# Kernel optimization log

Measured on AMD Instinct MI355X. Metric: run time of the kernel, lower is better.

Reference implementation:

```python
import jax, jax.numpy as jnp
import numpy as np

B, L, D, H = 2, 2048, 2048, 16
DH = D // H  # 128 per-head dim
EPS = 1e-5


def setup_inputs() -> dict:
    key = jax.random.key(0)
    ks = jax.random.split(key, 6)
    s = 0.02  # xavier-ish init scale with gain 2**-2.5
    return {
        "hidden_states": jax.random.normal(ks[0], (B, L, D), jnp.float32),
        "Wq": jax.random.normal(ks[1], (D, D), jnp.float32) * s,
        "Wk": jax.random.normal(ks[2], (D, D), jnp.float32) * s,
        "Wv": jax.random.normal(ks[3], (D, D), jnp.float32) * s,
        "Wb": jax.random.normal(ks[4], (D, H), jnp.float32) * s,
        "o_norm_weight": jnp.ones((DH,), jnp.float32),
        "Wo": jax.random.normal(ks[5], (D, D), jnp.float32) * s,
    }


def _delta_rule(q, k, v, beta):
    """Recurrent delta-rule linear attention.
    q,k,v: [B,H,L,Dh]; beta: [B,H,L]. Math identical to fused_chunk_delta_rule.
    S_t = S_{t-1} + k_t (beta_t * (v_t - S_{t-1}^T k_t))^T ;  o_t = S_t^T q_t
    """
    def step(S, inp):
        qt, kt, vt, bt = inp  # [B,H,Dh],[B,H,Dh],[B,H,Dh],[B,H]
        v_pred = jnp.einsum('bhk,bhkv->bhv', kt, S)
        delta = (vt - v_pred) * bt[..., None]
        S = S + kt[..., None] * delta[:, :, None, :]
        ot = jnp.einsum('bhk,bhkv->bhv', qt, S)
        return S, ot

    xs = (q.transpose(2, 0, 1, 3), k.transpose(2, 0, 1, 3),
          v.transpose(2, 0, 1, 3), beta.transpose(2, 0, 1))
    S0 = jnp.zeros(q.shape[:2] + (q.shape[-1], v.shape[-1]), q.dtype)
    _, o = jax.lax.scan(step, S0, xs)  # o: [L,B,H,Dh]
    return o.transpose(1, 2, 0, 3)  # [B,H,L,Dh]


def reference(hidden_states, Wq, Wk, Wv, Wb, o_norm_weight, Wo):
    b, l, d = hidden_states.shape
    h = Wb.shape[1]
    dh = d // h

    q = hidden_states @ Wq
    k = hidden_states @ Wk
    v = jax.nn.silu(hidden_states @ Wv)

    def heads(x):
        return x.reshape(b, l, h, dh).transpose(0, 2, 1, 3)  # b h l d

    q, k, v = heads(q), heads(k), heads(v)

    # qk_norm = 'l2' (torch F.normalize with eps clamp)
    def l2n(x):
        n = jnp.sqrt(jnp.sum(x * x, axis=-1, keepdims=True))
        return x / jnp.maximum(n, 1e-12)

    q, k = l2n(q), l2n(k)
    q = q * (dh ** -0.5)  # fla delta-rule default scale

    beta = jax.nn.sigmoid(hidden_states @ Wb).transpose(0, 2, 1)  # b h l

    o = _delta_rule(q, k, v, beta)  # b h l dh
    o = o.transpose(0, 2, 1, 3)  # b l h dh

    # RMSNorm over head_v_dim
    o = o * jax.lax.rsqrt(jnp.mean(o * o, axis=-1, keepdims=True) + EPS)
    o = o * o_norm_weight

    return o.reshape(b, l, d) @ Wo
```

## Files before the change

### kernel.cpp

```cpp
#include <hip/hip_runtime.h>
#include <hip/hip_bf16.h>
#include <cstdint>

#define DEV static __device__ __forceinline__

typedef unsigned short u16;
typedef unsigned int u32;
typedef __attribute__((ext_vector_type(8))) short short8;
typedef __attribute__((ext_vector_type(4))) float f32x4;

constexpr int Bn = 2, Ln = 2048, Dn = 2048, Hn = 16;
constexpr int Mrows = Bn * Ln;
constexpr int CHK = 64, NCK = Ln / CHK;
constexpr int NCHUNKS = Bn * Hn * NCK;

DEV float b2f(u16 s) { union { float f; u32 u; } x; x.u = ((u32)s) << 16; return x.f; }
DEV u16 f2b(float f) {
  union { float f; u32 u; } x; x.f = f; u32 u = x.u;
  return (u16)((u + 0x7fffu + ((u >> 16) & 1u)) >> 16);
}

DEV void cp16(const void* g, void* l) {
  __builtin_amdgcn_global_load_lds(
      (const __attribute__((address_space(1))) u32*)(unsigned long long)(g),
      (__attribute__((address_space(3))) u32*)(unsigned long long)(l), 16, 0, 0);
}

DEV f32x4 mfma16(short8 a, short8 b, f32x4 c) {
  return __builtin_amdgcn_mfma_f32_16x16x32_bf16(a, b, c, 0, 0, 0);
}

__global__ void k_cvt(const float* __restrict__ src, u16* __restrict__ dst, int n8) {
  int i = blockIdx.x * blockDim.x + threadIdx.x;
  if (i >= n8) return;
  const float4* s4 = (const float4*)(src + (size_t)i * 8);
  float4 a = s4[0], b = s4[1];
  u16 o[8] = {f2b(a.x), f2b(a.y), f2b(a.z), f2b(a.w), f2b(b.x), f2b(b.y), f2b(b.z), f2b(b.w)};
  *(short8*)(dst + (size_t)i * 8) = *(short8*)o;
}

struct TransArgs {
  const float* src[5]; u16* dst[5]; int rows[5]; int cols[5];
};
__global__ void k_trans(TransArgs t) {
  __shared__ u16 tile[32][33];
  int z = blockIdx.z;
  const float* src = t.src[z]; u16* dst = t.dst[z];
  int rows = t.rows[z], cols = t.cols[z];
  int r0 = blockIdx.y * 32, c0 = blockIdx.x * 32;
  if (r0 >= rows || c0 >= cols) return;
  int tx = threadIdx.x, ty = threadIdx.y;
  for (int i = ty; i < 32; i += 8) {
    int r = r0 + i, c = c0 + tx;
    if (r < rows && c < cols) tile[i][tx] = f2b(src[(size_t)r * cols + c]);
  }
  __syncthreads();
  for (int i = ty; i < 32; i += 8) {
    int r = c0 + i, c = r0 + tx;
    if (r < cols && c < rows) dst[(size_t)r * rows + c] = tile[tx][i];
  }
}

__global__ __launch_bounds__(256) void k_beta(const u16* __restrict__ hs,
                                              const u16* __restrict__ WbT,
                                              float* __restrict__ beta_g) {
  __shared__ float part[256];
  int tid = threadIdx.x, wave = tid >> 6, lane = tid & 63, quad = lane >> 4, l15 = lane & 15;
  int tok0 = blockIdx.x * 16;
  const u16* arow = hs + (size_t)(tok0 + l15) * Dn + wave * 512;
  const u16* brow = WbT + (size_t)l15 * Dn + wave * 512;
  f32x4 acc = {0.f, 0.f, 0.f, 0.f};
#pragma unroll
  for (int k = 0; k < 512; k += 32) {
    short8 af = *(const short8*)&arow[k + quad * 8];
    short8 bf = *(const short8*)&brow[k + quad * 8];
    acc = mfma16(af, bf, acc);
  }
  part[tid] = 0.f;
  __syncthreads();
#pragma unroll
  for (int r = 0; r < 4; r++) atomicAdd(&part[l15 * 16 + quad * 4 + r], acc[r]);
  __syncthreads();
  int h = tid >> 4, tr = tid & 15;
  int b = tok0 >> 11;
  int l = (tok0 + tr) & 2047;
  beta_g[(size_t)(b * Hn + h) * Ln + l] = 1.f / (1.f + __expf(-part[h * 16 + tr]));
}

struct Gemm2Args { const u16* A; const u16* Bt; u16* C; int K; };

__global__ __launch_bounds__(512, 2) void k_gemm2(Gemm2Args g) {
  __shared__ u16 ldsbuf[61440];
  const char* LB = (const char*)ldsbuf;
  const int K = g.K, NT = K / 64;
  const size_t Kb = (size_t)K * 2;
  int tid = threadIdx.x, wave = tid >> 6, lane = tid & 63;
  int quad = lane >> 4, l15 = lane & 15;
  int wm = wave >> 2, wn = wave & 3;

  int bid = blockIdx.x;
  int wg = (bid & 7) * 32 + (bid >> 3);
  int by = wg >> 4, bx = wg & 15;
  int m0 = by * 256, n0f = bx * 384;

  int r0 = tid >> 2;
  int cby = (((tid & 3) ^ ((tid >> 3) & 3)) * 16);
  const char* gA = (const char*)g.A + (size_t)(m0 + r0) * Kb + cby;
  const char* gB = (const char*)g.Bt + (size_t)(n0f + r0) * Kb + cby;

  auto stageA = [&](int slot, int t, int kh) {
    const char* src = gA + (size_t)t * 128 + kh * 64;
    u16* dst = &ldsbuf[slot * 8192 + tid * 8];
    cp16(src, dst);
    cp16(src + (size_t)128 * Kb, dst + 4096);
  };
  auto stageB = [&](int slot, int t, int kh) {
    const char* src = gB + (size_t)t * 128 + kh * 64;
    u16* dst = &ldsbuf[24576 + slot * 12288 + tid * 8];
    cp16(src, dst);
    cp16(src + (size_t)128 * Kb, dst + 4096);
    cp16(src + (size_t)256 * Kb, dst + 8192);
  };

  f32x4 acc0[4][6], acc1[4][6];
#pragma unroll
  for (int i = 0; i < 4; i++)
#pragma unroll
    for (int j = 0; j < 6; j++) {
      acc0[i][j] = (f32x4){0.f, 0.f, 0.f, 0.f};
      acc1[i][j] = (f32x4){0.f, 0.f, 0.f, 0.f};
    }

  int rsw = (l15 >> 1) & 3;
  int rA = (wm * 128 + l15) * 64 + ((quad ^ rsw) * 16);
  int rB = (wn * 96 + l15) * 64 + ((quad ^ rsw) * 16);

  stageA(0, 0, 0);
  stageB(0, 0, 0);
  stageA(1, 0, 1);
  stageB(1, 0, 1);

  short8 bf[6];
  int u0 = 0;
  for (int t = 0; t < NT; ++t) {
    int u1 = u0 + 1; if (u1 == 3) u1 = 0;
    int u2 = u1 + 1; if (u2 == 3) u2 = 0;
    bool pf = (t + 1 < NT);
    const char* aK0 = LB + u0 * 16384;
    const char* aK1 = LB + u1 * 16384;
    const char* bK0 = LB + 49152 + u0 * 24576;
    const char* bK1 = LB + 49152 + u1 * 24576;

    asm volatile("s_waitcnt vmcnt(5)" ::: "memory");
    __builtin_amdgcn_s_barrier();
    __builtin_amdgcn_sched_barrier(0);
    if (pf) stageA(u2, t + 1, 0);
    {
      short8 av[4];
#pragma unroll
      for (int i = 0; i < 4; i++) av[i] = *(const short8*)(aK0 + rA + i * 1024);
#pragma unroll
      for (int j = 0; j < 6; j++) bf[j] = *(const short8*)(bK0 + rB + j * 1024);
      __builtin_amdgcn_s_setprio(1);
#pragma unroll
      for (int i = 0; i < 4; i++)
#pragma unroll
        for (int j = 0; j < 6; j++) acc0[i][j] = mfma16(av[i], bf[j], acc0[i][j]);
      __builtin_amdgcn_s_setprio(0);
    }

    asm volatile("s_waitcnt vmcnt(5)" ::: "memory");
    __builtin_amdgcn_s_barrier();
    __builtin_amdgcn_sched_barrier(0);
    if (pf) stageB(u2, t + 1, 0);
    {
      short8 av[4];
#pragma unroll
      for (int i = 0; i < 4; i++) av[i] = *(const short8*)(aK0 + rA + 4096 + i * 1024);
      __builtin_amdgcn_s_setprio(1);
#pragma unroll
      for (int i = 0; i < 4; i++)
#pragma unroll
        for (int j = 0; j < 6; j++) acc1[i][j] = mfma16(av[i], bf[j], acc1[i][j]);
      __builtin_amdgcn_s_setprio(0);
    }

    if (t == NT - 1) asm volatile("s_waitcnt vmcnt(0)" ::: "memory");
    else asm volatile("s_waitcnt vmcnt(5)" ::: "memory");
    __builtin_amdgcn_s_barrier();
    __builtin_amdgcn_sched_barrier(0);
    if (pf) stageA(u0, t + 1, 1);
    {
      short8 av[4];
#pragma unroll
      for (int i = 0; i < 4; i++) av[i] = *(const short8*)(aK1 + rA + i * 1024);
#pragma unroll
      for (int j = 0; j < 6; j++) bf[j] = *(const short8*)(bK1 + rB + j * 1024);
      __builtin_amdgcn_s_setprio(1);
#pragma unroll
      for (int i = 0; i < 4; i++)
#pragma unroll
        for (int j = 0; j < 6; j++) acc0[i][j] = mfma16(av[i], bf[j], acc0[i][j]);
      __builtin_amdgcn_s_setprio(0);
    }

    asm volatile("s_waitcnt vmcnt(5)" ::: "memory");
    __builtin_amdgcn_s_barrier();
    __builtin_amdgcn_sched_barrier(0);
    if (pf) stageB(u0, t + 1, 1);
    {
      short8 av[4];
#pragma unroll
      for (int i = 0; i < 4; i++) av[i] = *(const short8*)(aK1 + rA + 4096 + i * 1024);
      __builtin_amdgcn_s_setprio(1);
#pragma unroll
      for (int i = 0; i < 4; i++)
#pragma unroll
        for (int j = 0; j < 6; j++) acc1[i][j] = mfma16(av[i], bf[j], acc1[i][j]);
      __builtin_amdgcn_s_setprio(0);
    }

    u0 = u2;
  }

#pragma unroll
  for (int mq = 0; mq < 2; mq++) {
#pragma unroll
    for (int i = 0; i < 4; i++)
#pragma unroll
      for (int j = 0; j < 6; j++) {
        f32x4 a = mq ? acc1[i][j] : acc0[i][j];
        int row = m0 + wm * 128 + mq * 64 + i * 16 + quad * 4;
        int colg = n0f + wn * 96 + j * 16;
        int z = colg >> 11;
        u16* Cz = g.C + (size_t)z * ((size_t)Mrows * 2048);
        int col = (colg & 2047) + l15;
#pragma unroll
        for (int r = 0; r < 4; r++) {
          float v = a[r];
          if (z == 2) v = v / (1.f + __expf(-v));
          Cz[(size_t)(row + r) * 2048 + col] = f2b(v);
        }
      }
  }
}

struct GemmoArgs { const u16* A; const u16* Bt; float* C; int K; };

__global__ __launch_bounds__(512, 2) void k_gemmo(GemmoArgs g) {
  __shared__ u16 ldsbuf[36864];
  const char* LB = (const char*)ldsbuf;
  const int K = g.K, NT = K / 64;
  const size_t Kb = (size_t)K * 2;
  int tid = threadIdx.x, wave = tid >> 6, lane = tid & 63;
  int quad = lane >> 4, l15 = lane & 15;
  int wm = wave >> 2, wn = wave & 3;

  int bid = blockIdx.x;
  int wg = (bid & 7) * 32 + (bid >> 3);
  int bx = wg >> 5, by = wg & 31;
  int m0 = by * 128, n0 = bx * 256;

  int r0 = tid >> 2;
  int cby = (((tid & 3) ^ ((tid >> 3) & 3)) * 16);
  const char* gA = (const char*)g.A + (size_t)(m0 + r0) * Kb + cby;
  const char* gB = (const char*)g.Bt + (size_t)(n0 + r0) * Kb + cby;

  auto stageA = [&](int slot, int t, int kh) {
    const char* src = gA + (size_t)t * 128 + kh * 64;
    cp16(src, &ldsbuf[slot * 4096 + tid * 8]);
  };
  auto stageB = [&](int slot, int t, int kh) {
    const char* src = gB + (size_t)t * 128 + kh * 64;
    u16* dst = &ldsbuf[12288 + slot * 8192 + tid * 8];
    cp16(src, dst);
    cp16(src + (size_t)128 * Kb, dst + 4096);
  };

  f32x4 acc[4][4];
#pragma unroll
  for (int i = 0; i < 4; i++)
#pragma unroll
    for (int j = 0; j < 4; j++) acc[i][j] = (f32x4){0.f, 0.f, 0.f, 0.f};

  int rsw = (l15 >> 1) & 3;
  int rA = (wm * 64 + l15) * 64 + ((quad ^ rsw) * 16);
  int rB = (wn * 64 + l15) * 64 + ((quad ^ rsw) * 16);

  stageA(0, 0, 0);
  stageB(0, 0, 0);
  stageA(1, 0, 1);
  stageB(1, 0, 1);

  short8 av[4];
  int u0 = 0;
  for (int t = 0; t < NT; ++t) {
    int u1 = u0 + 1; if (u1 == 3) u1 = 0;
    int u2 = u1 + 1; if (u2 == 3) u2 = 0;
    bool pf = (t + 1 < NT);
    const char* aK0 = LB + u0 * 8192;
    const char* aK1 = LB + u1 * 8192;
    const char* bK0 = LB + 24576 + u0 * 16384;
    const char* bK1 = LB + 24576 + u1 * 16384;

    asm volatile("s_waitcnt vmcnt(3)" ::: "memory");
    __builtin_amdgcn_s_barrier();
    __builtin_amdgcn_sched_barrier(0);
    if (pf) stageA(u2, t + 1, 0);
    {
      short8 bv[2];
#pragma unroll
      for (int i = 0; i < 4; i++) av[i] = *(const short8*)(aK0 + rA + i * 1024);
#pragma unroll
      for (int j = 0; j < 2; j++) bv[j] = *(const short8*)(bK0 + rB + j * 1024);
      __builtin_amdgcn_s_setprio(1);
#pragma unroll
      for (int i = 0; i < 4; i++)
#pragma unroll
        for (int j = 0; j < 2; j++) acc[i][j] = mfma16(av[i], bv[j], acc[i][j]);
      __builtin_amdgcn_s_setprio(0);
    }

    asm volatile("s_waitcnt vmcnt(3)" ::: "memory");
    __builtin_amdgcn_s_barrier();
    __builtin_amdgcn_sched_barrier(0);
    if (pf) stageB(u2, t + 1, 0);
    {
      short8 bv[2];
#pragma unroll
      for (int j = 0; j < 2; j++) bv[j] = *(const short8*)(bK0 + rB + (2 + j) * 1024);
      __builtin_amdgcn_s_setprio(1);
#pragma unroll
      for (int i = 0; i < 4; i++)
#pragma unroll
        for (int j = 0; j < 2; j++) acc[i][2 + j] = mfma16(av[i], bv[j], acc[i][2 + j]);
      __builtin_amdgcn_s_setprio(0);
    }

    if (t == NT - 1) asm volatile("s_waitcnt vmcnt(0)" ::: "memory");
    else asm volatile("s_waitcnt vmcnt(3)" ::: "memory");
    __builtin_amdgcn_s_barrier();
    __builtin_amdgcn_sched_barrier(0);
    if (pf) stageA(u0, t + 1, 1);
    {
      short8 bv[2];
#pragma unroll
      for (int i = 0; i < 4; i++) av[i] = *(const short8*)(aK1 + rA + i * 1024);
#pragma unroll
      for (int j = 0; j < 2; j++) bv[j] = *(const short8*)(bK1 + rB + j * 1024);
      __builtin_amdgcn_s_setprio(1);
#pragma unroll
      for (int i = 0; i < 4; i++)
#pragma unroll
        for (int j = 0; j < 2; j++) acc[i][j] = mfma16(av[i], bv[j], acc[i][j]);
      __builtin_amdgcn_s_setprio(0);
    }

    asm volatile("s_waitcnt vmcnt(3)" ::: "memory");
    __builtin_amdgcn_s_barrier();
    __builtin_amdgcn_sched_barrier(0);
    if (pf) stageB(u0, t + 1, 1);
    {
      short8 bv[2];
#pragma unroll
      for (int j = 0; j < 2; j++) bv[j] = *(const short8*)(bK1 + rB + (2 + j) * 1024);
      __builtin_amdgcn_s_setprio(1);
#pragma unroll
      for (int i = 0; i < 4; i++)
#pragma unroll
        for (int j = 0; j < 2; j++) acc[i][2 + j] = mfma16(av[i], bv[j], acc[i][2 + j]);
      __builtin_amdgcn_s_setprio(0);
    }

    u0 = u2;
  }

#pragma unroll
  for (int i = 0; i < 4; i++)
#pragma unroll
    for (int j = 0; j < 4; j++) {
      int row = m0 + wm * 64 + i * 16 + quad * 4;
      int col = n0 + wn * 64 + j * 16 + l15;
#pragma unroll
      for (int r = 0; r < 4; r++)
        g.C[(size_t)(row + r) * 2048 + col] = acc[i][j][r];
    }
}

__global__ void k_l2(u16* qn, u16* kn) {
  int tid = threadIdx.x, wave = tid >> 6, lane = tid & 63;
  size_t row = (size_t)blockIdx.x * 4 + wave;
  u16* p = (blockIdx.y ? kn : qn) + row * 128;
  u32 u = *(const u32*)&p[lane * 2];
  float x0 = b2f((u16)(u & 0xffff)), x1 = b2f((u16)(u >> 16));
  float ss = x0 * x0 + x1 * x1;
#pragma unroll
  for (int o = 32; o > 0; o >>= 1) ss += __shfl_xor(ss, o, 64);
  float sc = 1.f / fmaxf(sqrtf(ss), 1e-12f);
  if (blockIdx.y == 0) sc *= 0.08838834764831845f;
  u32 outv = (u32)f2b(x0 * sc) | ((u32)f2b(x1 * sc) << 16);
  *(u32*)&p[lane * 2] = outv;
}

constexpr int ST = 72;
__global__ __launch_bounds__(256, 4) void k_pre(
    const float* __restrict__ beta_g,
    const u16* __restrict__ qn, const u16* __restrict__ kn, const u16* __restrict__ vn,
    u16* __restrict__ W2g, u16* __restrict__ Ug, u16* __restrict__ Gg, u16* __restrict__ KTg) {
  __shared__ float beta_s[64];
  __shared__ u16 mats[4 * 64 * ST];
  int gid = blockIdx.x;
  int c = gid & 31, h = (gid >> 5) & 15, b = gid >> 9;
  int tid = threadIdx.x;
  int l0 = c * 64;

  if (tid < 64) beta_s[tid] = beta_g[(size_t)(b * Hn + h) * Ln + l0 + tid];
  __syncthreads();

  int wave = tid >> 6, lane = tid & 63, quad = lane >> 4, l15 = lane & 15;
  u16 *Br = mats, *Bc = mats + 64 * ST, *M0 = mats + 2 * 64 * ST, *M1 = mats + 3 * 64 * ST;

  {
    const u16* krowB = kn + (size_t)(b * Ln + l0 + wave * 16 + l15) * Dn + h * 128;
    short8 bfr[4];
#pragma unroll
    for (int s = 0; s < 4; s++) bfr[s] = *(const short8*)&krowB[quad * 8 + 32 * s];
#pragma unroll
    for (int mt = 0; mt < 4; ++mt) {
      const u16* arow_k = kn + (size_t)(b * Ln + l0 + mt * 16 + l15) * Dn + h * 128;
      const u16* arow_q = qn + (size_t)(b * Ln + l0 + mt * 16 + l15) * Dn + h * 128;
      f32x4 accA = {0.f, 0.f, 0.f, 0.f}, accG = {0.f, 0.f, 0.f, 0.f};
#pragma unroll
      for (int s = 0; s < 4; s++) {
        short8 ak = *(const short8*)&arow_k[quad * 8 + 32 * s];
        short8 aq = *(const short8*)&arow_q[quad * 8 + 32 * s];
        accA = mfma16(ak, bfr[s], accA);
        accG = mfma16(aq, bfr[s], accG);
      }
      int t = wave * 16 + l15;
#pragma unroll
      for (int r = 0; r < 4; r++) {
        int i = mt * 16 + quad * 4 + r;
        u16 nb = f2b((t < i) ? -beta_s[i] * accA[r] : 0.f);
        Br[i * ST + t] = nb;
        Bc[t * ST + i] = nb;
        M0[i * ST + t] = (t == i) ? f2b(1.f) : nb;
        Gg[(size_t)gid * 4096 + (size_t)i * 64 + t] = f2b((t <= i) ? accG[r] : 0.f);
      }
    }
  }
  __syncthreads();

  u16 *Mc = M0, *Mn = M1;
#pragma unroll
  for (int it = 0; it < 5; ++it) {
    const int tT = (it < 3) ? 0 : ((it == 3) ? 1 : 2);
    const int tI = (it < 4) ? 0 : 1;
    short8 bb[2];
#pragma unroll
    for (int s = 0; s < 2; s++) bb[s] = *(const short8*)&Bc[(wave * 16 + l15) * ST + quad * 8 + 32 * s];
    f32x4 accT[4];
#pragma unroll
    for (int mt = 0; mt < 4; mt++) {
      accT[mt] = (f32x4){0.f, 0.f, 0.f, 0.f};
      if (mt - wave >= tT) {
#pragma unroll
        for (int s = 0; s < 2; s++) {
          short8 af = *(const short8*)&Br[(mt * 16 + l15) * ST + quad * 8 + 32 * s];
          accT[mt] = mfma16(af, bb[s], accT[mt]);
        }
      }
    }
    __syncthreads();
#pragma unroll
    for (int mt = 0; mt < 4; mt++) {
      if (mt - wave >= tI) {
#pragma unroll
        for (int r = 0; r < 4; r++) {
          int i = mt * 16 + quad * 4 + r, t = wave * 16 + l15;
          u16 v = f2b(accT[mt][r]);
          Br[i * ST + t] = v;
          Bc[t * ST + i] = v;
        }
      }
    }
    __syncthreads();
    short8 tb[2];
#pragma unroll
    for (int s = 0; s < 2; s++) tb[s] = *(const short8*)&Bc[(wave * 16 + l15) * ST + quad * 8 + 32 * s];
#pragma unroll
    for (int mt = 0; mt < 4; mt++) {
      if (mt - wave >= tT) {
        f32x4 a;
#pragma unroll
        for (int r = 0; r < 4; r++) a[r] = b2f(Mc[(mt * 16 + quad * 4 + r) * ST + wave * 16 + l15]);
#pragma unroll
        for (int s = 0; s < 2; s++) {
          short8 af = *(const short8*)&Mc[(mt * 16 + l15) * ST + quad * 8 + 32 * s];
          a = mfma16(af, tb[s], a);
        }
#pragma unroll
        for (int r = 0; r < 4; r++) Mn[(mt * 16 + quad * 4 + r) * ST + wave * 16 + l15] = f2b(a[r]);
      } else {
#pragma unroll
        for (int r = 0; r < 4; r++)
          Mn[(mt * 16 + quad * 4 + r) * ST + wave * 16 + l15] =
              Mc[(mt * 16 + quad * 4 + r) * ST + wave * 16 + l15];
      }
    }
    u16* tmp = Mc; Mc = Mn; Mn = tmp;
  }
  __syncthreads();

  u16* XT = mats;
  u16* Mb = Mn;
  for (int idx = tid; idx < 512; idx += 256) {
    int i = idx >> 3, t8 = (idx & 7) * 8;
    short8 m8 = *(const short8*)&Mc[i * ST + t8];
    short8 o8;
#pragma unroll
    for (int e = 0; e < 8; e++) o8[e] = (short)f2b(b2f((u16)m8[e]) * beta_s[t8 + e]);
    *(short8*)&Mb[i * ST + t8] = o8;
  }
  int tv = tid & 63, dk0 = (tid >> 6) * 32;
  for (int pass = 0; pass < 2; ++pass) {
    const u16* src = pass ? vn : kn;
    const u16* srow = src + (size_t)(b * Ln + l0 + tv) * Dn + h * 128 + dk0;
#pragma unroll
    for (int s = 0; s < 4; s++) {
      short8 vv = *(const short8*)&srow[s * 8];
#pragma unroll
      for (int e = 0; e < 8; e++) XT[(dk0 + s * 8 + e) * ST + tv] = (u16)vv[e];
    }
    __syncthreads();
    if (pass == 0) {
#pragma unroll
      for (int it2 = 0; it2 < 4; it2++) {
        int idx = tid + it2 * 256;
        int dk = idx >> 3, t0 = (idx & 7) * 8;
        *(short8*)&KTg[(size_t)gid * 8192 + dk * 64 + t0] =
            *(const short8*)&XT[dk * ST + t0];
      }
    }
    u16* dst = pass ? Ug : W2g;
#pragma unroll
    for (int half = 0; half < 2; ++half) {
      int nt = wave + half * 4;
      short8 bx[2];
#pragma unroll
      for (int s = 0; s < 2; s++) bx[s] = *(const short8*)&XT[(nt * 16 + l15) * ST + quad * 8 + 32 * s];
#pragma unroll
      for (int mt = 0; mt < 4; mt++) {
        f32x4 a = {0.f, 0.f, 0.f, 0.f};
#pragma unroll
        for (int s = 0; s < 2; s++) {
          short8 af = *(const short8*)&Mb[(mt * 16 + l15) * ST + quad * 8 + 32 * s];
          a = mfma16(af, bx[s], a);
        }
#pragma unroll
        for (int r = 0; r < 4; r++)
          dst[(size_t)gid * 8192 + (size_t)(mt * 16 + quad * 4 + r) * 128 + nt * 16 + l15] = f2b(a[r]);
      }
    }
    __syncthreads();
  }
}

struct Frg { short8 w2[4], qf[4], gf[2], k0[2], k1[2]; float u[4]; };

__global__ __launch_bounds__(256) void k_scan(
    const u16* __restrict__ qn, const u16* __restrict__ W2g, const u16* __restrict__ Ug,
    const u16* __restrict__ Gg, const u16* __restrict__ KTg, u16* __restrict__ Og) {
  constexpr int SST = 136, DST = 104;
  __shared__ u16 Sb[16 * SST];
  __shared__ u16 Db[16 * DST];
  int bh = blockIdx.x, sl = blockIdx.y;
  int b = bh >> 4, h = bh & 15, c0 = sl * 16;
  int tid = threadIdx.x, wave = tid >> 6, lane = tid & 63, quad = lane >> 4, l15 = lane & 15;
  for (int i = tid; i < 16 * SST; i += 256) Sb[i] = 0;
  f32x4 accS0 = {0.f, 0.f, 0.f, 0.f}, accS1 = {0.f, 0.f, 0.f, 0.f};
  __syncthreads();

  auto load_frags = [&](Frg& F, int ci) {
    size_t ck = (size_t)bh * NCK + ci;
    const u16* w2row = W2g + ck * 8192 + (size_t)(wave * 16 + l15) * 128;
    const u16* qrow = qn + (size_t)(b * Ln + ci * 64 + wave * 16 + l15) * Dn + h * 128;
#pragma unroll
    for (int s = 0; s < 4; s++) {
      F.w2[s] = *(const short8*)&w2row[quad * 8 + 32 * s];
      F.qf[s] = *(const short8*)&qrow[quad * 8 + 32 * s];
    }
    const u16* grow = Gg + ck * 4096 + (size_t)(wave * 16 + l15) * 64;
    const u16* kt0 = KTg + ck * 8192 + (size_t)(wave * 16 + l15) * 64;
    const u16* kt1 = KTg + ck * 8192 + (size_t)((wave + 4) * 16 + l15) * 64;
#pragma unroll
    for (int s = 0; s < 2; s++) {
      F.gf[s] = *(const short8*)&grow[quad * 8 + 32 * s];
      F.k0[s] = *(const short8*)&kt0[quad * 8 + 32 * s];
      F.k1[s] = *(const short8*)&kt1[quad * 8 + 32 * s];
    }
    const u16* urow = Ug + ck * 8192 + (size_t)(wave * 16 + quad * 4) * 128 + c0 + l15;
#pragma unroll
    for (int r = 0; r < 4; r++) F.u[r] = b2f(urow[(size_t)r * 128]);
  };

  auto compute = [&](const Frg& F, int ci) {
    f32x4 accT = {0.f, 0.f, 0.f, 0.f}, accO = {0.f, 0.f, 0.f, 0.f};
#pragma unroll
    for (int s = 0; s < 4; s++) {
      short8 sf = *(const short8*)&Sb[l15 * SST + quad * 8 + 32 * s];
      accT = mfma16(F.w2[s], sf, accT);
      accO = mfma16(F.qf[s], sf, accO);
    }
#pragma unroll
    for (int r = 0; r < 4; r++) {
      float d = F.u[r] - accT[r];
      Db[l15 * DST + wave * 16 + quad * 4 + r] = f2b(d);
    }
    __syncthreads();
#pragma unroll
    for (int s = 0; s < 2; s++) {
      short8 df = *(const short8*)&Db[l15 * DST + quad * 8 + 32 * s];
      accO = mfma16(F.gf[s], df, accO);
      accS0 = mfma16(F.k0[s], df, accS0);
      accS1 = mfma16(F.k1[s], df, accS1);
    }
    u16* orow = Og + (size_t)(b * Ln + ci * 64 + wave * 16 + quad * 4) * Dn + h * 128 + c0 + l15;
#pragma unroll
    for (int r = 0; r < 4; r++) orow[(size_t)r * Dn] = f2b(accO[r]);
#pragma unroll
    for (int r = 0; r < 4; r++) {
      Sb[l15 * SST + wave * 16 + quad * 4 + r] = f2b(accS0[r]);
      Sb[l15 * SST + (wave + 4) * 16 + quad * 4 + r] = f2b(accS1[r]);
    }
    __syncthreads();
  };

  Frg FA, FB;
  load_frags(FA, 0);
  for (int ci = 0; ci < NCK; ci += 2) {
    load_frags(FB, ci + 1);
    compute(FA, ci);
    if (ci + 2 < NCK) load_frags(FA, ci + 2);
    compute(FB, ci + 1);
  }
}

__global__ void k_rms(const u16* __restrict__ Og, const float* __restrict__ w, u16* __restrict__ out) {
  int tid = threadIdx.x, wave = tid >> 6, lane = tid & 63;
  size_t row = (size_t)blockIdx.x * 4 + wave;
  const u16* p = Og + row * 128;
  u32 u = *(const u32*)&p[lane * 2];
  float x0 = b2f((u16)(u & 0xffff)), x1 = b2f((u16)(u >> 16));
  float ss = x0 * x0 + x1 * x1;
#pragma unroll
  for (int o = 32; o > 0; o >>= 1) ss += __shfl_xor(ss, o, 64);
  float sc = rsqrtf(ss * (1.f / 128.f) + 1e-5f);
  float w0 = w[lane * 2], w1 = w[lane * 2 + 1];
  u32 o2 = (u32)f2b(x0 * sc * w0) | ((u32)f2b(x1 * sc * w1) << 16);
  *(u32*)&out[row * 128 + lane * 2] = o2;
}

extern "C" void kernel_launch(void* const* d_in, const int* in_sizes, int n_in,
                              void* d_out, int out_size, void* d_ws, size_t ws_size,
                              hipStream_t stream) {
  (void)in_sizes; (void)n_in; (void)out_size; (void)ws_size;
  const float* hs_f = (const float*)d_in[0];
  const float* Wq = (const float*)d_in[1];
  const float* Wk = (const float*)d_in[2];
  const float* Wv = (const float*)d_in[3];
  const float* Wb = (const float*)d_in[4];
  const float* onw = (const float*)d_in[5];
  const float* Wo = (const float*)d_in[6];

  char* ws = (char*)d_ws;
  size_t off = 0;
  auto alloc = [&](size_t bytes) -> void* {
    void* p = ws + off;
    off += (bytes + 255) & ~(size_t)255;
    return p;
  };
  const size_t WB = (size_t)2048 * 2048 * 2;
  const size_t XB = (size_t)4096 * 2048 * 2;
  u16* WqT = (u16*)alloc(WB);
  u16* WkT = (u16*)alloc(WB);
  u16* WvT = (u16*)alloc(WB);
  u16* WoT = (u16*)alloc(WB);
  u16* WbT = (u16*)alloc((size_t)16 * 2048 * 2);
  u16* hsb = (u16*)alloc(XB);
  u16* qn  = (u16*)alloc(XB);
  u16* kn  = (u16*)alloc(XB);
  u16* vn  = (u16*)alloc(XB);
  u16* W2g = (u16*)alloc((size_t)NCHUNKS * 8192 * 2);
  u16* Ug  = (u16*)alloc((size_t)NCHUNKS * 8192 * 2);
  u16* Gg  = (u16*)alloc((size_t)NCHUNKS * 4096 * 2);
  u16* KTg = (u16*)alloc((size_t)NCHUNKS * 8192 * 2);
  float* beta_g = (float*)alloc((size_t)Bn * Hn * Ln * 4);
  u16* Og = vn;
  u16* onorm = qn;

  hipLaunchKernelGGL(k_cvt, dim3(Mrows * Dn / 8 / 256), dim3(256), 0, stream, hs_f, hsb, Mrows * Dn / 8);

  TransArgs ta;
  ta.src[0] = Wq; ta.dst[0] = WqT; ta.rows[0] = 2048; ta.cols[0] = 2048;
  ta.src[1] = Wk; ta.dst[1] = WkT; ta.rows[1] = 2048; ta.cols[1] = 2048;
  ta.src[2] = Wv; ta.dst[2] = WvT; ta.rows[2] = 2048; ta.cols[2] = 2048;
  ta.src[3] = Wo; ta.dst[3] = WoT; ta.rows[3] = 2048; ta.cols[3] = 2048;
  ta.src[4] = Wb; ta.dst[4] = WbT; ta.rows[4] = 2048; ta.cols[4] = 16;
  hipLaunchKernelGGL(k_trans, dim3(64, 64, 5), dim3(32, 8), 0, stream, ta);

  hipLaunchKernelGGL(k_beta, dim3(Mrows / 16), dim3(256), 0, stream, hsb, WbT, beta_g);

  {
    Gemm2Args g2;
    g2.A = hsb; g2.Bt = WqT; g2.C = qn; g2.K = 2048;
    hipLaunchKernelGGL(k_gemm2, dim3(256), dim3(512), 0, stream, g2);
  }

  hipLaunchKernelGGL(k_l2, dim3(16384, 2), dim3(256), 0, stream, qn, kn);

  hipLaunchKernelGGL(k_pre, dim3(NCHUNKS), dim3(256), 0, stream,
                     beta_g, qn, kn, vn, W2g, Ug, Gg, KTg);

  hipLaunchKernelGGL(k_scan, dim3(32, 8), dim3(256), 0, stream,
                     qn, W2g, Ug, Gg, KTg, Og);

  hipLaunchKernelGGL(k_rms, dim3(16384), dim3(256), 0, stream, Og, onw, onorm);

  {
    GemmoArgs go;
    go.A = onorm; go.Bt = WoT; go.C = (float*)d_out; go.K = 2048;
    hipLaunchKernelGGL(k_gemmo, dim3(256), dim3(512), 0, stream, go);
  }
}
```

Before: 446.7 us.

## Fuse L2 norm into chunk preprocessing and vectorize weight transposes

Removes the standalone k_l2 kernel: k_pre now computes per-row L2 norms of q and k, scales fragments on the fly, and writes a chunk-contiguous normalized Q buffer that k_scan reads. It also replaces the 32x32 scalar transpose of the four square weights with a 64x64-tile kernel using float4 loads and 16-byte stores, keeping the old kernel only for Wb. This removes one read-modify-write pass over q and k and makes the weight conversion cheaper. In exchange it adds redundant rescaling work inside k_pre, an extra Q buffer write, and an LDS column read in the new transpose that may hit bank conflicts.

```diff
diff --git a/kernel.cpp b/kernel.cpp
--- a/kernel.cpp
+++ b/kernel.cpp
@@ -28,6 +28,13 @@
 
 DEV f32x4 mfma16(short8 a, short8 b, f32x4 c) {
   return __builtin_amdgcn_mfma_f32_16x16x32_bf16(a, b, c, 0, 0, 0);
+}
+
+DEV short8 scale8(short8 v, float sc) {
+  short8 o;
+#pragma unroll
+  for (int e = 0; e < 8; e++) o[e] = (short)f2b(b2f((u16)v[e]) * sc);
+  return o;
 }
 
 __global__ void k_cvt(const float* __restrict__ src, u16* __restrict__ dst, int n8) {
@@ -39,14 +46,40 @@
   *(short8*)(dst + (size_t)i * 8) = *(short8*)o;
 }
 
+struct Trans2Args { const float* src[4]; u16* dst[4]; };
+__global__ __launch_bounds__(256) void k_trans2(Trans2Args t) {
+  __shared__ u16 tile[64][72];
+  const float* src = t.src[blockIdx.z];
+  u16* dst = t.dst[blockIdx.z];
+  int r0 = blockIdx.y * 64, c0 = blockIdx.x * 64;
+  int tid = threadIdx.x;
+  int lr = tid >> 2, lc = (tid & 3) * 16;
+  const float* s = src + (size_t)(r0 + lr) * 2048 + c0 + lc;
+#pragma unroll
+  for (int i = 0; i < 4; i++) {
+    float4 v = *(const float4*)(s + i * 4);
+    tile[lr][lc + i * 4 + 0] = f2b(v.x);
+    tile[lr][lc + i * 4 + 1] = f2b(v.y);
+    tile[lr][lc + i * 4 + 2] = f2b(v.z);
+    tile[lr][lc + i * 4 + 3] = f2b(v.w);
+  }
+  __syncthreads();
+  int orr = tid >> 2, oc = (tid & 3) * 16;
+  u16* d = dst + (size_t)(c0 + orr) * 2048 + r0 + oc;
+  u16 buf[16];
+#pragma unroll
+  for (int e = 0; e < 16; e++) buf[e] = tile[oc + e][orr];
+  *(short8*)(d) = *(short8*)buf;
+  *(short8*)(d + 8) = *(short8*)(buf + 8);
+}
+
 struct TransArgs {
-  const float* src[5]; u16* dst[5]; int rows[5]; int cols[5];
+  const float* src[1]; u16* dst[1]; int rows[1]; int cols[1];
 };
 __global__ void k_trans(TransArgs t) {
   __shared__ u16 tile[32][33];
-  int z = blockIdx.z;
-  const float* src = t.src[z]; u16* dst = t.dst[z];
-  int rows = t.rows[z], cols = t.cols[z];
+  const float* src = t.src[0]; u16* dst = t.dst[0];
+  int rows = t.rows[0], cols = t.cols[0];
   int r0 = blockIdx.y * 32, c0 = blockIdx.x * 32;
   if (r0 >= rows || c0 >= cols) return;
   int tx = threadIdx.x, ty = threadIdx.y;
@@ -387,53 +420,65 @@
     }
 }
 
-__global__ void k_l2(u16* qn, u16* kn) {
-  int tid = threadIdx.x, wave = tid >> 6, lane = tid & 63;
-  size_t row = (size_t)blockIdx.x * 4 + wave;
-  u16* p = (blockIdx.y ? kn : qn) + row * 128;
-  u32 u = *(const u32*)&p[lane * 2];
-  float x0 = b2f((u16)(u & 0xffff)), x1 = b2f((u16)(u >> 16));
-  float ss = x0 * x0 + x1 * x1;
-#pragma unroll
-  for (int o = 32; o > 0; o >>= 1) ss += __shfl_xor(ss, o, 64);
-  float sc = 1.f / fmaxf(sqrtf(ss), 1e-12f);
-  if (blockIdx.y == 0) sc *= 0.08838834764831845f;
-  u32 outv = (u32)f2b(x0 * sc) | ((u32)f2b(x1 * sc) << 16);
-  *(u32*)&p[lane * 2] = outv;
-}
-
 constexpr int ST = 72;
 __global__ __launch_bounds__(256, 4) void k_pre(
     const float* __restrict__ beta_g,
     const u16* __restrict__ qn, const u16* __restrict__ kn, const u16* __restrict__ vn,
-    u16* __restrict__ W2g, u16* __restrict__ Ug, u16* __restrict__ Gg, u16* __restrict__ KTg) {
+    u16* __restrict__ W2g, u16* __restrict__ Ug, u16* __restrict__ Gg, u16* __restrict__ KTg,
+    u16* __restrict__ Qg) {
   __shared__ float beta_s[64];
+  __shared__ float rnk_s[64], rnq_s[64];
   __shared__ u16 mats[4 * 64 * ST];
   int gid = blockIdx.x;
   int c = gid & 31, h = (gid >> 5) & 15, b = gid >> 9;
   int tid = threadIdx.x;
   int l0 = c * 64;
 
+  int wave = tid >> 6, lane = tid & 63, quad = lane >> 4, l15 = lane & 15;
+  u16 *Br = mats, *Bc = mats + 64 * ST, *M0 = mats + 2 * 64 * ST, *M1 = mats + 3 * 64 * ST;
+
+  short8 bfr[4], qfr[4];
+  {
+    int row = wave * 16 + l15;
+    const u16* krow = kn + (size_t)(b * Ln + l0 + row) * Dn + h * 128;
+    const u16* qrow = qn + (size_t)(b * Ln + l0 + row) * Dn + h * 128;
+    float ssk = 0.f, ssq = 0.f;
+#pragma unroll
+    for (int s = 0; s < 4; s++) {
+      bfr[s] = *(const short8*)&krow[quad * 8 + 32 * s];
+      qfr[s] = *(const short8*)&qrow[quad * 8 + 32 * s];
+#pragma unroll
+      for (int e = 0; e < 8; e++) {
+        float xk = b2f((u16)bfr[s][e]), xq = b2f((u16)qfr[s][e]);
+        ssk += xk * xk; ssq += xq * xq;
+      }
+    }
+    ssk += __shfl_xor(ssk, 16, 64); ssk += __shfl_xor(ssk, 32, 64);
+    ssq += __shfl_xor(ssq, 16, 64); ssq += __shfl_xor(ssq, 32, 64);
+    float rk = 1.f / fmaxf(sqrtf(ssk), 1e-12f);
+    float rq = 0.08838834764831845f / fmaxf(sqrtf(ssq), 1e-12f);
+    if (quad == 0) { rnk_s[row] = rk; rnq_s[row] = rq; }
+#pragma unroll
+    for (int s = 0; s < 4; s++) {
+      bfr[s] = scale8(bfr[s], rk);
+      *(short8*)&Qg[(size_t)gid * 8192 + (size_t)row * 128 + quad * 8 + 32 * s] =
+          scale8(qfr[s], rq);
+    }
+  }
   if (tid < 64) beta_s[tid] = beta_g[(size_t)(b * Hn + h) * Ln + l0 + tid];
   __syncthreads();
 
-  int wave = tid >> 6, lane = tid & 63, quad = lane >> 4, l15 = lane & 15;
-  u16 *Br = mats, *Bc = mats + 64 * ST, *M0 = mats + 2 * 64 * ST, *M1 = mats + 3 * 64 * ST;
-
   {
-    const u16* krowB = kn + (size_t)(b * Ln + l0 + wave * 16 + l15) * Dn + h * 128;
-    short8 bfr[4];
-#pragma unroll
-    for (int s = 0; s < 4; s++) bfr[s] = *(const short8*)&krowB[quad * 8 + 32 * s];
 #pragma unroll
     for (int mt = 0; mt < 4; ++mt) {
       const u16* arow_k = kn + (size_t)(b * Ln + l0 + mt * 16 + l15) * Dn + h * 128;
       const u16* arow_q = qn + (size_t)(b * Ln + l0 + mt * 16 + l15) * Dn + h * 128;
+      float rkA = rnk_s[mt * 16 + l15], rqA = rnq_s[mt * 16 + l15];
       f32x4 accA = {0.f, 0.f, 0.f, 0.f}, accG = {0.f, 0.f, 0.f, 0.f};
 #pragma unroll
       for (int s = 0; s < 4; s++) {
-        short8 ak = *(const short8*)&arow_k[quad * 8 + 32 * s];
-        short8 aq = *(const short8*)&arow_q[quad * 8 + 32 * s];
+        short8 ak = scale8(*(const short8*)&arow_k[quad * 8 + 32 * s], rkA);
+        short8 aq = scale8(*(const short8*)&arow_q[quad * 8 + 32 * s], rqA);
         accA = mfma16(ak, bfr[s], accA);
         accG = mfma16(aq, bfr[s], accG);
       }
@@ -526,9 +571,11 @@
   for (int pass = 0; pass < 2; ++pass) {
     const u16* src = pass ? vn : kn;
     const u16* srow = src + (size_t)(b * Ln + l0 + tv) * Dn + h * 128 + dk0;
+    float rsc = pass ? 1.f : rnk_s[tv];
 #pragma unroll
     for (int s = 0; s < 4; s++) {
       short8 vv = *(const short8*)&srow[s * 8];
+      if (!pass) vv = scale8(vv, rsc);
 #pragma unroll
       for (int e = 0; e < 8; e++) XT[(dk0 + s * 8 + e) * ST + tv] = (u16)vv[e];
     }
@@ -569,7 +616,7 @@
 struct Frg { short8 w2[4], qf[4], gf[2], k0[2], k1[2]; float u[4]; };
 
 __global__ __launch_bounds__(256) void k_scan(
-    const u16* __restrict__ qn, const u16* __restrict__ W2g, const u16* __restrict__ Ug,
+    const u16* __restrict__ Qg, const u16* __restrict__ W2g, const u16* __restrict__ Ug,
     const u16* __restrict__ Gg, const u16* __restrict__ KTg, u16* __restrict__ Og) {
   constexpr int SST = 136, DST = 104;
   __shared__ u16 Sb[16 * SST];
@@ -584,7 +631,7 @@
   auto load_frags = [&](Frg& F, int ci) {
     size_t ck = (size_t)bh * NCK + ci;
     const u16* w2row = W2g + ck * 8192 + (size_t)(wave * 16 + l15) * 128;
-    const u16* qrow = qn + (size_t)(b * Ln + ci * 64 + wave * 16 + l15) * Dn + h * 128;
+    const u16* qrow = Qg + ck * 8192 + (size_t)(wave * 16 + l15) * 128;
 #pragma unroll
     for (int s = 0; s < 4; s++) {
       F.w2[s] = *(const short8*)&w2row[quad * 8 + 32 * s];
@@ -695,19 +742,22 @@
   u16* Ug  = (u16*)alloc((size_t)NCHUNKS * 8192 * 2);
   u16* Gg  = (u16*)alloc((size_t)NCHUNKS * 4096 * 2);
   u16* KTg = (u16*)alloc((size_t)NCHUNKS * 8192 * 2);
+  u16* Qg  = (u16*)alloc((size_t)NCHUNKS * 8192 * 2);
   float* beta_g = (float*)alloc((size_t)Bn * Hn * Ln * 4);
   u16* Og = vn;
   u16* onorm = qn;
 
   hipLaunchKernelGGL(k_cvt, dim3(Mrows * Dn / 8 / 256), dim3(256), 0, stream, hs_f, hsb, Mrows * Dn / 8);
 
+  Trans2Args t2;
+  t2.src[0] = Wq; t2.dst[0] = WqT;
+  t2.src[1] = Wk; t2.dst[1] = WkT;
+  t2.src[2] = Wv; t2.dst[2] = WvT;
+  t2.src[3] = Wo; t2.dst[3] = WoT;
+  hipLaunchKernelGGL(k_trans2, dim3(32, 32, 4), dim3(256), 0, stream, t2);
   TransArgs ta;
-  ta.src[0] = Wq; ta.dst[0] = WqT; ta.rows[0] = 2048; ta.cols[0] = 2048;
-  ta.src[1] = Wk; ta.dst[1] = WkT; ta.rows[1] = 2048; ta.cols[1] = 2048;
-  ta.src[2] = Wv; ta.dst[2] = WvT; ta.rows[2] = 2048; ta.cols[2] = 2048;
-  ta.src[3] = Wo; ta.dst[3] = WoT; ta.rows[3] = 2048; ta.cols[3] = 2048;
-  ta.src[4] = Wb; ta.dst[4] = WbT; ta.rows[4] = 2048; ta.cols[4] = 16;
-  hipLaunchKernelGGL(k_trans, dim3(64, 64, 5), dim3(32, 8), 0, stream, ta);
+  ta.src[0] = Wb; ta.dst[0] = WbT; ta.rows[0] = 2048; ta.cols[0] = 16;
+  hipLaunchKernelGGL(k_trans, dim3(1, 64, 1), dim3(32, 8), 0, stream, ta);
 
   hipLaunchKernelGGL(k_beta, dim3(Mrows / 16), dim3(256), 0, stream, hsb, WbT, beta_g);
 
@@ -717,13 +767,11 @@
     hipLaunchKernelGGL(k_gemm2, dim3(256), dim3(512), 0, stream, g2);
   }
 
-  hipLaunchKernelGGL(k_l2, dim3(16384, 2), dim3(256), 0, stream, qn, kn);
-
   hipLaunchKernelGGL(k_pre, dim3(NCHUNKS), dim3(256), 0, stream,
-                     beta_g, qn, kn, vn, W2g, Ug, Gg, KTg);
+                     beta_g, qn, kn, vn, W2g, Ug, Gg, KTg, Qg);
 
   hipLaunchKernelGGL(k_scan, dim3(32, 8), dim3(256), 0, stream,
-                     qn, W2g, Ug, Gg, KTg, Og);
+                     Qg, W2g, Ug, Gg, KTg, Og);
 
   hipLaunchKernelGGL(k_rms, dim3(16384), dim3(256), 0, stream, Og, onw, onorm);
 
```

Result: faster. 418.1 us (-6.4%).
